# Kernel tuning notes

Hardware: AMD Instinct MI355X
Metric: run time of the kernel (lower is better)

## Reference

```python
import jax, jax.numpy as jnp
import numpy as np

B, T, V, E, H, C = 128, 256, 50000, 300, 512, 11
START, STOP = 9, 10
NEG = -100000.0


def _lstm_dir(x, mask, w_ih, w_hh, b_ih, b_hh, reverse):
    # x: [B,T,D]; precompute input-to-gate projection for all timesteps
    gx = jnp.einsum('btd,gd->btg', x, w_ih) + b_ih + b_hh
    m = mask
    if reverse:
        gx = gx[:, ::-1]
        m = m[:, ::-1]
    Bc = x.shape[0]
    Hh = w_hh.shape[1]

    def step(carry, inp):
        h, c = carry
        g, mt = inp
        gates = g + h @ w_hh.T  # [B,4H]
        i, f, gg, o = jnp.split(gates, 4, axis=-1)
        i = jax.nn.sigmoid(i)
        f = jax.nn.sigmoid(f)
        o = jax.nn.sigmoid(o)
        gg = jnp.tanh(gg)
        c_new = f * c + i * gg
        h_new = o * jnp.tanh(c_new)
        mt = mt[:, None]
        h = jnp.where(mt, h_new, h)  # packed-sequence semantics: hold state on pads
        c = jnp.where(mt, c_new, c)
        return (h, c), h

    init = (jnp.zeros((Bc, Hh), x.dtype), jnp.zeros((Bc, Hh), x.dtype))
    _, hs = jax.lax.scan(step, init, (gx.transpose(1, 0, 2), m.T))
    hs = hs.transpose(1, 0, 2)
    if reverse:
        hs = hs[:, ::-1]
    # pad_packed_sequence zeroes padded positions
    return hs * mask[..., None].astype(x.dtype)


def _encode(tokens, mask, embeddings, params):
    x = embeddings[tokens]
    for (wif, whf, bif, bhf, wir, whr, bir, bhr) in params:
        fwd = _lstm_dir(x, mask, wif, whf, bif, bhf, False)
        bwd = _lstm_dir(x, mask, wir, whr, bir, bhr, True)
        x = jnp.concatenate([fwd, bwd], -1)
    return x


def _viterbi(emis, mask, transitions, seq_len):
    def vstep(scores, inp):
        emi, mt = inp
        cand = scores[:, :, None] + transitions[None]  # [B,C,C]
        bt = jnp.argmax(cand, axis=1)
        new = jnp.max(cand, axis=1) + emi
        return jnp.where(mt[:, None], new, scores), bt

    scores0 = jnp.zeros_like(emis[:, 0, :])
    final, backtrack = jax.lax.scan(vstep, scores0, (emis.transpose(1, 0, 2), mask.T))
    final = final + transitions[:, STOP][None]
    best_last = jnp.argmax(final, axis=-1)  # [B]

    ls = jnp.arange(emis.shape[1] - 1, -1, -1)

    def btstep(cur, inp):
        bt_l, l = inp
        emit = jnp.where(l < seq_len, cur, 0)  # pad tail with 0 as in original
        prev = jnp.take_along_axis(bt_l, cur[:, None], axis=1)[:, 0]
        cur = jnp.where((l >= 1) & (l <= seq_len - 1), prev, cur)
        return cur, emit

    _, emits = jax.lax.scan(btstep, best_last, (backtrack[::-1], ls))
    return emits[::-1].T  # [B,T]


def _nll(emis, tags, mask, transitions, seq_len):
    # CRF forward algorithm (replicates original init with -1e5 full scores)
    def fstep(scores, inp):
        emi, mt = inp
        new = jax.nn.logsumexp(scores[:, :, None] + emi[:, None, :] + transitions[None], axis=1)
        return jnp.where(mt[:, None], new, scores), None

    scores0 = jnp.full_like(emis[:, 0, :], NEG)
    final, _ = jax.lax.scan(fstep, scores0, (emis.transpose(1, 0, 2), mask.T))
    fwd_score = jax.nn.logsumexp(final + transitions[:, STOP][None], axis=-1, keepdims=True)

    em_sc = jnp.take_along_axis(emis, tags[..., None], -1)[..., 0]  # [B,T]
    y_aug = jnp.concatenate([jnp.full((tags.shape[0], 1), START, tags.dtype), tags], 1)
    tr_sc = transitions[y_aug[:, :-1], y_aug[:, 1:]]  # [B,T]
    last_tag = jnp.take_along_axis(y_aug, seq_len[:, None], 1)
    last_tr = transitions[last_tag[:, 0], STOP][:, None]
    mf = mask.astype(emis.dtype)
    gold = (mf * (em_sc + tr_sc)).sum(-1, keepdims=True) + last_tr
    return (fwd_score - gold).mean()


def setup_inputs() -> dict:
    key = jax.random.key(0)
    ks = iter(jax.random.split(key, 40))
    sl = jax.random.randint(next(ks), (B,), 1, T + 1)
    sl = -jnp.sort(-sl.at[0].set(T))  # descending, max == T (pack_padded requirement)
    mask = jnp.arange(T)[None, :] < sl[:, None]
    tokens = jax.random.randint(next(ks), (B, T), 0, V)
    tags = jax.random.randint(next(ks), (B, T), 0, 9)
    s = 1.0 / float(np.sqrt(H))

    def u(shape):
        return jax.random.uniform(next(ks), shape, jnp.float32, -s, s)

    inp = dict(tokens=tokens, seq_len=sl, mask=mask, tags=tags,
               embeddings=jax.random.normal(next(ks), (V, E), jnp.float32) * 0.1)
    G = 4 * H
    for li, d in enumerate([E, 2 * H]):
        for suf in ['', 'r']:
            inp[f'w_ih_l{li}{suf}'] = u((G, d))
            inp[f'w_hh_l{li}{suf}'] = u((G, H))
            inp[f'b_ih_l{li}{suf}'] = u((G,))
            inp[f'b_hh_l{li}{suf}'] = u((G,))
    inp['fc_w'] = u((C, 2 * H))
    inp['fc_b'] = u((C,))
    tr = jax.random.normal(next(ks), (C, C), jnp.float32)
    inp['transitions'] = tr.at[START, :].set(-1.0).at[:, STOP].set(-1.0)
    return inp


def reference(tokens, seq_len, mask, tags, embeddings,
              w_ih_l0, w_hh_l0, b_ih_l0, b_hh_l0,
              w_ih_l0r, w_hh_l0r, b_ih_l0r, b_hh_l0r,
              w_ih_l1, w_hh_l1, b_ih_l1, b_hh_l1,
              w_ih_l1r, w_hh_l1r, b_ih_l1r, b_hh_l1r,
              fc_w, fc_b, transitions):
    params = [(w_ih_l0, w_hh_l0, b_ih_l0, b_hh_l0, w_ih_l0r, w_hh_l0r, b_ih_l0r, b_hh_l0r),
              (w_ih_l1, w_hh_l1, b_ih_l1, b_hh_l1, w_ih_l1r, w_hh_l1r, b_ih_l1r, b_hh_l1r)]
    out = _encode(tokens, mask, embeddings, params)  # [B,T,2H]
    emis = jnp.einsum('bth,ch->btc', out, fc_w) + fc_b  # CRF fc (dropout=eval no-op)
    pred = _viterbi(emis, mask, transitions, seq_len)
    loss = _nll(emis, tags, mask, transitions, seq_len)
    return pred, loss
```

## Files before the change

### kernel.cpp

```cpp
#include <hip/hip_runtime.h>
#include <hip/hip_bf16.h>
#include <hip/hip_fp16.h>

#define BB   128
#define TT   256
#define EE   300
#define KP0  320
#define HH   512
#define GG   2048
#define NC   11
#define MM   (BB*TT)
#define START_TAG 9
#define STOP_TAG  10
#define NEGV (-100000.0f)

typedef _Float16 h2_t __attribute__((ext_vector_type(2)));
typedef _Float16 h4_t __attribute__((ext_vector_type(4)));
typedef _Float16 h8_t __attribute__((ext_vector_type(8)));
typedef float    f4_t __attribute__((ext_vector_type(4)));

__device__ __forceinline__ float sigf(float x) { return 1.0f / (1.0f + __expf(-x)); }

__global__ __launch_bounds__(256) void init_kernel(float* out, int* flags) {
    int t = threadIdx.x;
    if (t == 0) out[MM] = 0.0f;
    for (int i = t; i < 1024; i += 256) flags[i] = 0;
}

__global__ __launch_bounds__(256) void conv_pad_kernel(const float* __restrict__ W,
                                                       _Float16* __restrict__ O,
                                                       int K, int Kp4, int total4) {
    int idx = blockIdx.x * 256 + threadIdx.x;
    if (idx >= total4) return;
    int r = idx / Kp4, c4 = idx % Kp4, c = c4 * 4;
    h4_t v;
    if (c < K) {
        float4 f = *(const float4*)(W + (size_t)r * K + c);
        v[0] = (_Float16)f.x; v[1] = (_Float16)f.y; v[2] = (_Float16)f.z; v[3] = (_Float16)f.w;
    } else {
        v[0] = v[1] = v[2] = v[3] = (_Float16)0.0f;
    }
    *(h4_t*)(O + (size_t)r * (Kp4 * 4) + c) = v;
}

__global__ __launch_bounds__(256) void embed16_kernel(const int* __restrict__ tok,
                                                      const float* __restrict__ emb,
                                                      _Float16* __restrict__ x0,
                                                      int total4) {
    int idx = blockIdx.x * 256 + threadIdx.x;
    if (idx >= total4) return;
    int m = idx / (KP0 / 4), c4 = idx % (KP0 / 4), c = c4 * 4;
    h4_t v;
    if (c < EE) {
        float4 f = *(const float4*)(emb + (size_t)tok[m] * EE + c);
        v[0] = (_Float16)f.x; v[1] = (_Float16)f.y; v[2] = (_Float16)f.z; v[3] = (_Float16)f.w;
    } else {
        v[0] = v[1] = v[2] = v[3] = (_Float16)0.0f;
    }
    *(h4_t*)(x0 + (size_t)m * KP0 + c) = v;
}

#define LDA 72
__global__ __launch_bounds__(256) void gemm_bt_kernel(const _Float16* __restrict__ A,
                                                      const _Float16* __restrict__ Wf,
                                                      const float* __restrict__ b1,
                                                      const float* __restrict__ b2,
                                                      _Float16* __restrict__ C,
                                                      int Kp) {
    __shared__ __align__(16) char smem[36864];
    _Float16* As = (_Float16*)smem;
    _Float16* Bs = (_Float16*)(smem + 18432);
    const int tid = threadIdx.x;
    const int m0 = blockIdx.y * 128, n0 = blockIdx.x * 128;
    const int wv = tid >> 6, lane = tid & 63;
    const int wm = wv & 1, wn = wv >> 1;
    const int col = lane & 15, quad = lane >> 4;

    f4_t acc[4][4];
#pragma unroll
    for (int i = 0; i < 4; ++i)
#pragma unroll
        for (int j = 0; j < 4; ++j) acc[i][j] = (f4_t){0.f, 0.f, 0.f, 0.f};

    for (int k0 = 0; k0 < Kp; k0 += 64) {
#pragma unroll
        for (int cch = 0; cch < 4; ++cch) {
            int id = cch * 256 + tid;
            int row = id >> 3, cc = id & 7;
            h8_t va = *(const h8_t*)(A + (size_t)(m0 + row) * Kp + k0 + cc * 8);
            h8_t vb = *(const h8_t*)(Wf + (size_t)(n0 + row) * Kp + k0 + cc * 8);
            *(h8_t*)(As + row * LDA + cc * 8) = va;
            *(h8_t*)(Bs + row * LDA + cc * 8) = vb;
        }
        __syncthreads();
#pragma unroll
        for (int kk = 0; kk < 2; ++kk) {
            h8_t af[4], bf[4];
#pragma unroll
            for (int i = 0; i < 4; ++i) {
                af[i] = *(const h8_t*)(As + (wm * 64 + i * 16 + col) * LDA + kk * 32 + quad * 8);
                bf[i] = *(const h8_t*)(Bs + (wn * 64 + i * 16 + col) * LDA + kk * 32 + quad * 8);
            }
#pragma unroll
            for (int mi = 0; mi < 4; ++mi)
#pragma unroll
                for (int ni = 0; ni < 4; ++ni)
                    acc[mi][ni] = __builtin_amdgcn_mfma_f32_16x16x32_f16(af[mi], bf[ni], acc[mi][ni], 0, 0, 0);
        }
        __syncthreads();
    }

    _Float16* Ct = (_Float16*)smem;
#pragma unroll
    for (int ni = 0; ni < 4; ++ni) {
        int n = n0 + wn * 64 + ni * 16 + col;
        float bias = b1[n] + b2[n];
#pragma unroll
        for (int mi = 0; mi < 4; ++mi) {
#pragma unroll
            for (int r = 0; r < 4; ++r) {
                int mrow = wm * 64 + mi * 16 + quad * 4 + r;
                Ct[mrow * 136 + wn * 64 + ni * 16 + col] = (_Float16)(acc[mi][ni][r] + bias);
            }
        }
    }
    __syncthreads();
    {
        int row = tid >> 1, half = tid & 1;
#pragma unroll
        for (int cc2 = 0; cc2 < 8; ++cc2) {
            h8_t v = *(const h8_t*)(Ct + row * 136 + half * 64 + cc2 * 8);
            *(h8_t*)(C + (size_t)(m0 + row) * GG + n0 + half * 64 + cc2 * 8) = v;
        }
    }
}

__global__ __launch_bounds__(256, 1) void lstm_rec3_kernel(
        const _Float16* __restrict__ gx_f, const _Float16* __restrict__ gx_r,
        const float* __restrict__ whh_f, const float* __restrict__ whh_r,
        const int* __restrict__ seqlen, int c0, int nbg,
        _Float16* __restrict__ hs, _Float16* __restrict__ hbuf, int* __restrict__ flags) {
    extern __shared__ _Float16 Wlds[];
    _Float16* hstage = Wlds + 32768;

    const int wg = blockIdx.x;
    const int gs = wg & 15;
    const int grp = wg >> 4;
    const int bg = grp % nbg;
    const int dir = grp / nbg;
    const _Float16* gx = dir ? gx_r : gx_f;
    const float* W = dir ? whh_r : whh_f;
    int* myFlags = flags + grp * 16;
    _Float16* hb = hbuf + (size_t)grp * 2 * 16384;

    const int tid = threadIdx.x;
    const int wv = tid >> 6, lane = tid & 63;
    const int mt = wv & 1;
    const int p  = wv >> 1;
    const int col = lane & 15, quad = lane >> 4;

    for (int e = tid; e < 4096; e += 256) {
        int ln = e & 63, kc = (e >> 6) & 15, nt = e >> 10;
        int pp = nt >> 1;
        int n_in_pair = ((nt & 1) << 4) + (ln & 15);
        int gt = n_in_pair >> 3, jj = n_in_pair & 7;
        int R = gt * 512 + gs * 16 + pp * 8 + jj;
        int k = kc * 32 + (ln >> 4) * 8;
        const float4* src = (const float4*)(W + (size_t)R * 512 + k);
        float4 f0 = src[0], f1 = src[1];
        h8_t v;
        v[0] = (_Float16)f0.x; v[1] = (_Float16)f0.y; v[2] = (_Float16)f0.z; v[3] = (_Float16)f0.w;
        v[4] = (_Float16)f1.x; v[5] = (_Float16)f1.y; v[6] = (_Float16)f1.z; v[7] = (_Float16)f1.w;
        *(h8_t*)(Wlds + (size_t)e * 8) = v;
    }
    __syncthreads();

    const int maxsl = seqlen[c0 + bg * 32];
    int sl_r[4];
#pragma unroll
    for (int r = 0; r < 4; ++r) sl_r[r] = seqlen[c0 + bg * 32 + mt * 16 + quad * 4 + r];

    const int jglob = gs * 16 + p * 8 + (col & 7);
    const int hi = col >> 3;

    _Float16 pg0[4], pg1[4];
#pragma unroll
    for (int r = 0; r < 4; ++r) {
        pg0[r] = (_Float16)0.0f; pg1[r] = (_Float16)0.0f;
        if (0 < sl_r[r]) {
            int tm = dir ? (sl_r[r] - 1) : 0;
            int b_loc = bg * 32 + mt * 16 + quad * 4 + r;
            size_t base = ((size_t)(b_loc * TT + tm)) * GG;
            pg0[r] = gx[base + hi * 512 + jglob];
            pg1[r] = gx[base + 1024 + hi * 512 + jglob];
        }
    }

    if (tid < 128) {
        int m = tid >> 2, q = tid & 3;
        unsigned long long z = 0ull;
        const _Float16* dst = hb + 16384 + m * 512 + gs * 16 + q * 4;
        asm volatile("global_store_dwordx2 %0, %1, off sc0 sc1" :: "v"(dst), "v"(z) : "memory");
    }
    asm volatile("s_waitcnt vmcnt(0)" ::: "memory");
    __syncthreads();
    if (tid == 0) {
        int one = 1;
        asm volatile("global_store_dword %0, %1, off sc0 sc1" :: "v"(myFlags + gs), "v"(one) : "memory");
    }

    float cst[4] = {0.f, 0.f, 0.f, 0.f};
    float hst[4] = {0.f, 0.f, 0.f, 0.f};

    for (int s = 0; s < maxsl; ++s) {
        if (tid < 16) {
            const int* fp = myFlags + tid;
            int v, it = 0;
            for (;;) {
                asm volatile("global_load_dword %0, %1, off sc0 sc1\n\ts_waitcnt vmcnt(0)"
                             : "=v"(v) : "v"(fp) : "memory");
                if (v >= s + 1) break;
                if (it < 3) __builtin_amdgcn_s_sleep(1);
                else        __builtin_amdgcn_s_sleep(4);
                ++it;
            }
        }
        __syncthreads();

        const _Float16* hrd = hb + ((s + 1) & 1) * 16384;
        _Float16* hwr = hb + (s & 1) * 16384;

        h8_t a[16];
        const _Float16* ap = hrd + (mt * 16 + col) * 512 + quad * 8;
#pragma unroll
        for (int kc = 0; kc < 16; ++kc)
            asm volatile("global_load_dwordx4 %0, %1, off sc0 sc1"
                         : "=v"(a[kc]) : "v"(ap + kc * 32));
        asm volatile("s_waitcnt vmcnt(0)" ::: "memory");

        f4_t acc0 = {0.f, 0.f, 0.f, 0.f};
        f4_t acc1 = {0.f, 0.f, 0.f, 0.f};
#pragma unroll
        for (int kc = 0; kc < 16; ++kc) {
            h8_t b0 = *(const h8_t*)(Wlds + (((p * 2 + 0) * 16 + kc) * 64 + lane) * 8);
            h8_t b1 = *(const h8_t*)(Wlds + (((p * 2 + 1) * 16 + kc) * 64 + lane) * 8);
            acc0 = __builtin_amdgcn_mfma_f32_16x16x32_f16(a[kc], b0, acc0, 0, 0, 0);
            acc1 = __builtin_amdgcn_mfma_f32_16x16x32_f16(a[kc], b1, acc1, 0, 0, 0);
        }

#pragma unroll
        for (int r = 0; r < 4; ++r) {
            const bool valid = (s < sl_r[r]);
            float a0 = acc0[r] + (float)pg0[r];
            float a1 = acc1[r] + (float)pg1[r];
            float x0v = __shfl_xor(a0, 8);
            float x1v = __shfl_xor(a1, 8);
            float gi = hi ? x0v : a0;
            float gf = hi ? a0 : x0v;
            float gg2 = hi ? x1v : a1;
            float go = hi ? a1 : x1v;
            if (valid) {
                float cn = sigf(gf) * cst[r] + sigf(gi) * tanhf(gg2);
                cst[r] = cn;
                hst[r] = sigf(go) * tanhf(cn);
            }
            if (!hi)
                hstage[(mt * 16 + quad * 4 + r) * 16 + p * 8 + (col & 7)] = (_Float16)hst[r];
        }
        __syncthreads();

        if (tid < 128) {
            int m = tid >> 2, q = tid & 3;
            unsigned long long v = *(const unsigned long long*)(hstage + m * 16 + q * 4);
            const _Float16* dst = hwr + m * 512 + gs * 16 + q * 4;
            asm volatile("global_store_dwordx2 %0, %1, off sc0 sc1" :: "v"(dst), "v"(v) : "memory");
        }
        asm volatile("s_waitcnt vmcnt(0)" ::: "memory");
        __syncthreads();
        if (tid == 0) {
            int fv = s + 2;
            asm volatile("global_store_dword %0, %1, off sc0 sc1" :: "v"(myFlags + gs), "v"(fv) : "memory");
        }

#pragma unroll
        for (int r = 0; r < 4; ++r) {
            const bool valid = (s < sl_r[r]);
            if (valid && !hi) {
                int b_loc = bg * 32 + mt * 16 + quad * 4 + r;
                int tm = dir ? (sl_r[r] - 1 - s) : s;
                hs[((size_t)(b_loc * TT + tm) << 10) + (dir << 9) + jglob] = (_Float16)hst[r];
            }
        }
        {
            int sn = s + 1;
#pragma unroll
            for (int r = 0; r < 4; ++r) {
                pg0[r] = (_Float16)0.0f; pg1[r] = (_Float16)0.0f;
                if (sn < sl_r[r]) {
                    int tm = dir ? (sl_r[r] - 1 - sn) : sn;
                    int b_loc = bg * 32 + mt * 16 + quad * 4 + r;
                    size_t base = ((size_t)(b_loc * TT + tm)) * GG;
                    pg0[r] = gx[base + hi * 512 + jglob];
                    pg1[r] = gx[base + 1024 + hi * 512 + jglob];
                }
            }
        }
    }
}

__global__ __launch_bounds__(256) void emis_kernel(const _Float16* __restrict__ hs,
                                                   const float* __restrict__ fc_w,
                                                   const float* __restrict__ fc_b,
                                                   float* __restrict__ emis, int n) {
    int idx = blockIdx.x * 256 + threadIdx.x;
    if (idx >= n) return;
    int m = idx / NC, cc = idx % NC;
    const h8_t* a = (const h8_t*)(hs + (size_t)m * 1024);
    const float4* w = (const float4*)(fc_w + (size_t)cc * 1024);
    float s = 0.f;
#pragma unroll 4
    for (int k = 0; k < 128; ++k) {
        h8_t x = a[k];
        float4 y0 = w[2 * k], y1 = w[2 * k + 1];
        s += (float)x[0] * y0.x + (float)x[1] * y0.y + (float)x[2] * y0.z + (float)x[3] * y0.w;
        s += (float)x[4] * y1.x + (float)x[5] * y1.y + (float)x[6] * y1.z + (float)x[7] * y1.w;
    }
    emis[idx] = s + fc_b[cc];
}

__global__ __launch_bounds__(64) void crf_kernel(const float* __restrict__ emis,
                                                 const int* __restrict__ seq_len,
                                                 const int* __restrict__ tags,
                                                 const float* __restrict__ trans,
                                                 unsigned char* __restrict__ bt,
                                                 float* __restrict__ out, int c0) {
    const int b_loc = blockIdx.x;
    const int b = c0 + b_loc;
    const int lane = threadIdx.x;
    __shared__ float tr[NC * NC];
    for (int i = lane; i < NC * NC; i += 64) tr[i] = trans[i];
    __syncthreads();
    const int sl = seq_len[b];
    const bool act = lane < NC;
    const int jj = act ? lane : 0;

    float vs = 0.0f;
    float ns = NEGV;

    for (int t = 0; t < sl; ++t) {
        float ej = act ? emis[(size_t)(b_loc * TT + t) * NC + lane] : 0.0f;
        float vmax = -1e30f, nmax = -1e30f;
        int varg = 0;
        float nsave[NC];
#pragma unroll
        for (int i = 0; i < NC; ++i) {
            float vi = __shfl(vs, i);
            float ni = __shfl(ns, i);
            float tij = tr[i * NC + jj];
            float cv = vi + tij;
            if (cv > vmax) { vmax = cv; varg = i; }
            float cn = ni + tij;
            nsave[i] = cn;
            if (cn > nmax) nmax = cn;
        }
        float ssum = 0.f;
#pragma unroll
        for (int i = 0; i < NC; ++i) ssum += expf(nsave[i] - nmax);
        if (act) {
            vs = vmax + ej;
            ns = nmax + logf(ssum) + ej;
            bt[(size_t)(b_loc * TT + t) * NC + lane] = (unsigned char)varg;
        }
    }

    float finv = act ? vs + tr[lane * NC + STOP_TAG] : -1e30f;
    float finn = act ? ns + tr[lane * NC + STOP_TAG] : -1e30f;
    float vbest = -1e30f, fmax = -1e30f;
    int barg = 0;
#pragma unroll
    for (int j = 0; j < NC; ++j) {
        float v = __shfl(finv, j);
        if (v > vbest) { vbest = v; barg = j; }
        float n = __shfl(finn, j);
        if (n > fmax) fmax = n;
    }
    float fsum = 0.f;
#pragma unroll
    for (int j = 0; j < NC; ++j) fsum += expf(__shfl(finn, j) - fmax);
    float fwd = fmax + logf(fsum);

    float gsum = 0.f;
    for (int t = lane; t < sl; t += 64) {
        int tg = tags[b * TT + t];
        int pv = (t == 0) ? START_TAG : tags[b * TT + t - 1];
        gsum += emis[(size_t)(b_loc * TT + t) * NC + tg] + tr[pv * NC + tg];
    }
#pragma unroll
    for (int off = 32; off > 0; off >>= 1) gsum += __shfl_down(gsum, off);

    if (lane == 0) {
        float gold = gsum + tr[tags[b * TT + sl - 1] * NC + STOP_TAG];
        atomicAdd(out + MM, (fwd - gold) * (1.0f / (float)BB));
        int cur = barg;
        for (int l = sl - 1; l >= 0; --l) {
            out[b * TT + l] = (float)cur;
            if (l >= 1) cur = (int)bt[(size_t)(b_loc * TT + l) * NC + cur];
        }
    }
    for (int l = sl + lane; l < TT; l += 64) out[b * TT + l] = 0.0f;
}

extern "C" void kernel_launch(void* const* d_in, const int* in_sizes, int n_in,
                              void* d_out, int out_size, void* d_ws, size_t ws_size,
                              hipStream_t stream) {
    (void)in_sizes; (void)n_in; (void)out_size;
    const int* tokens = (const int*)d_in[0];
    const int* seqlen = (const int*)d_in[1];
    const int* tags = (const int*)d_in[3];
    const float* emb = (const float*)d_in[4];
    const float* w_ih_l0  = (const float*)d_in[5];
    const float* w_hh_l0  = (const float*)d_in[6];
    const float* b_ih_l0  = (const float*)d_in[7];
    const float* b_hh_l0  = (const float*)d_in[8];
    const float* w_ih_l0r = (const float*)d_in[9];
    const float* w_hh_l0r = (const float*)d_in[10];
    const float* b_ih_l0r = (const float*)d_in[11];
    const float* b_hh_l0r = (const float*)d_in[12];
    const float* w_ih_l1  = (const float*)d_in[13];
    const float* w_hh_l1  = (const float*)d_in[14];
    const float* b_ih_l1  = (const float*)d_in[15];
    const float* b_hh_l1  = (const float*)d_in[16];
    const float* w_ih_l1r = (const float*)d_in[17];
    const float* w_hh_l1r = (const float*)d_in[18];
    const float* b_ih_l1r = (const float*)d_in[19];
    const float* b_hh_l1r = (const float*)d_in[20];
    const float* fc_w  = (const float*)d_in[21];
    const float* fc_b  = (const float*)d_in[22];
    const float* trans = (const float*)d_in[23];

    const size_t per_b = 2097152u + 524288u + 163840u + 11264u + 2816u;
    const size_t fixed = 524288u + 4096u + 2u * 1310720u + 2u * 4194304u;
    int Bc = 128;
    while (Bc > 32 && fixed + per_b * (size_t)Bc > ws_size) Bc >>= 1;

    char* ws = (char*)d_ws;
    _Float16* hbuf = (_Float16*)ws;
    int* flags = (int*)(ws + 524288u);
    _Float16* w0f = (_Float16*)(ws + 528384u);
    _Float16* w0r = (_Float16*)(ws + 528384u + 1310720u);
    _Float16* w1f = (_Float16*)(ws + 528384u + 2u * 1310720u);
    _Float16* w1r = (_Float16*)(ws + 528384u + 2u * 1310720u + 4194304u);
    char* p = ws + fixed;
    _Float16* gxf   = (_Float16*)p;   p += (size_t)Bc * 1048576u;
    _Float16* gxr   = (_Float16*)p;   p += (size_t)Bc * 1048576u;
    _Float16* hs    = (_Float16*)p;   p += (size_t)Bc * 524288u;
    _Float16* x0f16 = (_Float16*)p;   p += (size_t)Bc * 163840u;
    float* emis     = (float*)p;      p += (size_t)Bc * 11264u;
    unsigned char* bt = (unsigned char*)p;
    float* out = (float*)d_out;

    init_kernel<<<1, 256, 0, stream>>>(out, flags);
    conv_pad_kernel<<<(2048 * 80 + 255) / 256, 256, 0, stream>>>(w_ih_l0,  w0f, EE, 80, 2048 * 80);
    conv_pad_kernel<<<(2048 * 80 + 255) / 256, 256, 0, stream>>>(w_ih_l0r, w0r, EE, 80, 2048 * 80);
    conv_pad_kernel<<<(2048 * 256 + 255) / 256, 256, 0, stream>>>(w_ih_l1,  w1f, 1024, 256, 2048 * 256);
    conv_pad_kernel<<<(2048 * 256 + 255) / 256, 256, 0, stream>>>(w_ih_l1r, w1r, 1024, 256, 2048 * 256);

    const int nbg = Bc / 32;
    const int nchunk = BB / Bc;
    for (int cidx = 0; cidx < nchunk; ++cidx) {
        const int c0 = cidx * Bc;
        const int Mc = Bc * TT;
        dim3 gdim(GG / 128, Mc / 128);
        int* fl_l0 = flags + (cidx * 2 + 0) * 128;
        int* fl_l1 = flags + (cidx * 2 + 1) * 128;

        embed16_kernel<<<(Mc * 80 + 255) / 256, 256, 0, stream>>>(tokens + c0 * TT, emb, x0f16, Mc * 80);
        gemm_bt_kernel<<<gdim, 256, 0, stream>>>(x0f16, w0f, b_ih_l0,  b_hh_l0,  gxf, KP0);
        gemm_bt_kernel<<<gdim, 256, 0, stream>>>(x0f16, w0r, b_ih_l0r, b_hh_l0r, gxr, KP0);
        lstm_rec3_kernel<<<2 * nbg * 16, 256, 66560, stream>>>(
            gxf, gxr, w_hh_l0, w_hh_l0r, seqlen, c0, nbg, hs, hbuf, fl_l0);
        gemm_bt_kernel<<<gdim, 256, 0, stream>>>(hs, w1f, b_ih_l1,  b_hh_l1,  gxf, 1024);
        gemm_bt_kernel<<<gdim, 256, 0, stream>>>(hs, w1r, b_ih_l1r, b_hh_l1r, gxr, 1024);
        lstm_rec3_kernel<<<2 * nbg * 16, 256, 66560, stream>>>(
            gxf, gxr, w_hh_l1, w_hh_l1r, seqlen, c0, nbg, hs, hbuf, fl_l1);
        emis_kernel<<<(Mc * NC + 255) / 256, 256, 0, stream>>>(hs, fc_w, fc_b, emis, Mc * NC);
        crf_kernel<<<Bc, 64, 0, stream>>>(emis, seqlen, tags, trans, bt, out, c0);
    }
}
```

Before: 5.772 ms.

## Keep recurrent weights in registers and shrink per-step publish barrier

Loads the recurrent-weight MFMA B fragments from LDS into registers once before the time loop instead of re-reading LDS every step. Splits the 16-deep MFMA accumulation chain into two independent chains to shorten the dependency latency. Publishes the new hidden slice with 64 threads using 16-byte stores confined to one wavefront, removing a block-wide __syncthreads before the flag store. This raises VGPR pressure (an extra 64 registers' worth of fragments) and relies on single-wave ordering of the store and the flag write.

```diff
diff --git a/kernel.cpp b/kernel.cpp
--- a/kernel.cpp
+++ b/kernel.cpp
@@ -175,6 +175,13 @@
     }
     __syncthreads();
 
+    h8_t Bf0[16], Bf1[16];
+#pragma unroll
+    for (int kc = 0; kc < 16; ++kc) {
+        Bf0[kc] = *(const h8_t*)(Wlds + (((p * 2 + 0) * 16 + kc) * 64 + lane) * 8);
+        Bf1[kc] = *(const h8_t*)(Wlds + (((p * 2 + 1) * 16 + kc) * 64 + lane) * 8);
+    }
+
     const int maxsl = seqlen[c0 + bg * 32];
     int sl_r[4];
 #pragma unroll
@@ -196,17 +203,16 @@
         }
     }
 
-    if (tid < 128) {
-        int m = tid >> 2, q = tid & 3;
-        unsigned long long z = 0ull;
-        const _Float16* dst = hb + 16384 + m * 512 + gs * 16 + q * 4;
-        asm volatile("global_store_dwordx2 %0, %1, off sc0 sc1" :: "v"(dst), "v"(z) : "memory");
-    }
-    asm volatile("s_waitcnt vmcnt(0)" ::: "memory");
-    __syncthreads();
-    if (tid == 0) {
-        int one = 1;
-        asm volatile("global_store_dword %0, %1, off sc0 sc1" :: "v"(myFlags + gs), "v"(one) : "memory");
+    if (tid < 64) {
+        int m = tid >> 1, half = tid & 1;
+        h8_t z = {};
+        const _Float16* dst = hb + 16384 + m * 512 + gs * 16 + half * 8;
+        asm volatile("global_store_dwordx4 %0, %1, off sc0 sc1" :: "v"(dst), "v"(z) : "memory");
+        asm volatile("s_waitcnt vmcnt(0)" ::: "memory");
+        if (tid == 0) {
+            int one = 1;
+            asm volatile("global_store_dword %0, %1, off sc0 sc1" :: "v"(myFlags + gs), "v"(one) : "memory");
+        }
     }
 
     float cst[4] = {0.f, 0.f, 0.f, 0.f};
@@ -237,16 +243,22 @@
             asm volatile("global_load_dwordx4 %0, %1, off sc0 sc1"
                          : "=v"(a[kc]) : "v"(ap + kc * 32));
         asm volatile("s_waitcnt vmcnt(0)" ::: "memory");
-
-        f4_t acc0 = {0.f, 0.f, 0.f, 0.f};
-        f4_t acc1 = {0.f, 0.f, 0.f, 0.f};
-#pragma unroll
-        for (int kc = 0; kc < 16; ++kc) {
-            h8_t b0 = *(const h8_t*)(Wlds + (((p * 2 + 0) * 16 + kc) * 64 + lane) * 8);
-            h8_t b1 = *(const h8_t*)(Wlds + (((p * 2 + 1) * 16 + kc) * 64 + lane) * 8);
-            acc0 = __builtin_amdgcn_mfma_f32_16x16x32_f16(a[kc], b0, acc0, 0, 0, 0);
-            acc1 = __builtin_amdgcn_mfma_f32_16x16x32_f16(a[kc], b1, acc1, 0, 0, 0);
-        }
+        __builtin_amdgcn_sched_barrier(0);
+
+        f4_t acc0a = {0.f, 0.f, 0.f, 0.f}, acc0b = {0.f, 0.f, 0.f, 0.f};
+        f4_t acc1a = {0.f, 0.f, 0.f, 0.f}, acc1b = {0.f, 0.f, 0.f, 0.f};
+#pragma unroll
+        for (int kc = 0; kc < 8; ++kc) {
+            acc0a = __builtin_amdgcn_mfma_f32_16x16x32_f16(a[kc], Bf0[kc], acc0a, 0, 0, 0);
+            acc1a = __builtin_amdgcn_mfma_f32_16x16x32_f16(a[kc], Bf1[kc], acc1a, 0, 0, 0);
+        }
+#pragma unroll
+        for (int kc = 8; kc < 16; ++kc) {
+            acc0b = __builtin_amdgcn_mfma_f32_16x16x32_f16(a[kc], Bf0[kc], acc0b, 0, 0, 0);
+            acc1b = __builtin_amdgcn_mfma_f32_16x16x32_f16(a[kc], Bf1[kc], acc1b, 0, 0, 0);
+        }
+        f4_t acc0 = acc0a + acc0b;
+        f4_t acc1 = acc1a + acc1b;
 
 #pragma unroll
         for (int r = 0; r < 4; ++r) {
@@ -269,17 +281,16 @@
         }
         __syncthreads();
 
-        if (tid < 128) {
-            int m = tid >> 2, q = tid & 3;
-            unsigned long long v = *(const unsigned long long*)(hstage + m * 16 + q * 4);
-            const _Float16* dst = hwr + m * 512 + gs * 16 + q * 4;
-            asm volatile("global_store_dwordx2 %0, %1, off sc0 sc1" :: "v"(dst), "v"(v) : "memory");
-        }
-        asm volatile("s_waitcnt vmcnt(0)" ::: "memory");
-        __syncthreads();
-        if (tid == 0) {
-            int fv = s + 2;
-            asm volatile("global_store_dword %0, %1, off sc0 sc1" :: "v"(myFlags + gs), "v"(fv) : "memory");
+        if (tid < 64) {
+            int m = tid >> 1, half = tid & 1;
+            h8_t v = *(const h8_t*)(hstage + m * 16 + half * 8);
+            const _Float16* dst = hwr + m * 512 + gs * 16 + half * 8;
+            asm volatile("global_store_dwordx4 %0, %1, off sc0 sc1" :: "v"(dst), "v"(v) : "memory");
+            asm volatile("s_waitcnt vmcnt(0)" ::: "memory");
+            if (tid == 0) {
+                int fv = s + 2;
+                asm volatile("global_store_dword %0, %1, off sc0 sc1" :: "v"(myFlags + gs), "v"(fv) : "memory");
+            }
         }
 
 #pragma unroll
```

New measurement: 5.300 ms. 8.2% less time.
